# Optimization experiments

Hardware: AMD Instinct MI355X
Metric: run time of the kernel (lower is better)

## Reference

```python
import jax, jax.numpy as jnp
import numpy as np

N_IN = 8192
C_IN, C_H, C_OUT = 64, 32, 32
L = 3
GRID = 64  # parent grid extent (parents live on even coords of a 128^3 grid)


def _build_coords_and_maps():
    """Build sparse voxel coords and the 27-offset kernel map for 3x3x3 stride-1 convs."""
    rng = np.random.RandomState(0)
    pts = rng.randint(0, GRID, size=(4 * N_IN, 3))
    uniq = np.unique(pts, axis=0)
    parents = uniq[rng.permutation(uniq.shape[0])[:N_IN]] * 2  # stride-2 coords in [0,128)
    offs = np.array([[i, j, k] for i in (0, 1) for j in (0, 1) for k in (0, 1)])
    # generative conv transpose kernel=2 stride=2: child k of parent i sits at row i*8+k
    coords = (parents[:, None, :] + offs[None]).reshape(-1, 3)
    n_out = coords.shape[0]
    D = 2 * GRID
    grid = -np.ones((D, D, D), dtype=np.int64)
    grid[coords[:, 0], coords[:, 1], coords[:, 2]] = np.arange(n_out)
    k_offs = np.array([[i, j, k] for i in (-1, 0, 1) for j in (-1, 0, 1) for k in (-1, 0, 1)])
    ins, outs = [], []
    for d in k_offs:
        sh = coords + d
        valid = np.all((sh >= 0) & (sh < D), axis=1)
        j = -np.ones(n_out, dtype=np.int64)
        j[valid] = grid[sh[valid, 0], sh[valid, 1], sh[valid, 2]]
        m = j >= 0
        ins.append(j[m])
        outs.append(np.nonzero(m)[0])
    P = max(len(a) for a in ins)
    nbr_in = np.full((27, P), n_out, dtype=np.int32)   # pad -> dummy zero row
    nbr_out = np.full((27, P), n_out, dtype=np.int32)  # pad -> dummy dropped row
    for k in range(27):
        nbr_in[k, : len(ins[k])] = ins[k]
        nbr_out[k, : len(outs[k])] = outs[k]
    return jnp.asarray(nbr_in), jnp.asarray(nbr_out), n_out


def setup_inputs() -> dict:
    nbr_in, nbr_out, n_out = _build_coords_and_maps()
    key = jax.random.key(0)
    ks = jax.random.split(key, 20)
    w = lambda k, shape, fan: jax.random.normal(k, shape, jnp.float32) / np.float32(np.sqrt(fan))
    C4, C2 = C_OUT // 4, C_OUT // 2
    inp = {
        "x": jax.random.normal(ks[0], (N_IN, C_IN), jnp.float32),
        "W_up": w(ks[1], (8, C_IN, C_H), C_IN),
        "b_up": 0.01 * jax.random.normal(ks[2], (C_H,), jnp.float32),
        "W_conv": w(ks[3], (27, C_H, C_OUT), 27 * C_H),
        "b_conv": 0.01 * jax.random.normal(ks[4], (C_OUT,), jnp.float32),
        "Wb00": w(ks[5], (L, 27, C_OUT, C4), 27 * C_OUT),
        "bb00": 0.01 * jax.random.normal(ks[6], (L, C4), jnp.float32),
        "Wb01": w(ks[7], (L, 27, C4, C2), 27 * C4),
        "bb01": 0.01 * jax.random.normal(ks[8], (L, C2), jnp.float32),
        "Wb10": w(ks[9], (L, C_OUT, C4), C_OUT),
        "bb10": 0.01 * jax.random.normal(ks[10], (L, C4), jnp.float32),
        "Wb11": w(ks[11], (L, 27, C4, C4), 27 * C4),
        "bb11": 0.01 * jax.random.normal(ks[12], (L, C4), jnp.float32),
        "Wb12": w(ks[13], (L, C4, C2), C4),
        "bb12": 0.01 * jax.random.normal(ks[14], (L, C2), jnp.float32),
        "W_cls": w(ks[15], (27, C_OUT, 1), 27 * C_OUT),
        "b_cls": 0.01 * jax.random.normal(ks[16], (1,), jnp.float32),
        "nbr_in": nbr_in,
        "nbr_out": nbr_out,
        # ground-truth occupancy of out coords in target_label (precomputed set membership)
        "target": jax.random.bernoulli(ks[17], 0.5, (n_out,)),
    }
    return inp


def reference(x, W_up, b_up, W_conv, b_conv, Wb00, bb00, Wb01, bb01,
              Wb10, bb10, Wb11, bb11, Wb12, bb12, W_cls, b_cls,
              nbr_in, nbr_out, target):
    n_out = target.shape[0]
    r = jax.nn.relu

    def sconv(f, W, b):
        # 3x3x3 stride-1 sparse conv via shared kernel map: gather -> per-offset GEMM -> scatter-add
        fpad = jnp.concatenate([f, jnp.zeros((1, f.shape[1]), f.dtype)], axis=0)
        g = fpad[nbr_in]                                   # [27, P, Cin]
        contrib = jnp.einsum('kpc,kcd->kpd', g, W)         # [27, P, Cout]
        out = jnp.zeros((n_out + 1, W.shape[2]), f.dtype)
        out = out.at[nbr_out.reshape(-1)].add(contrib.reshape(-1, W.shape[2]))
        return out[:n_out] + b

    # generative transpose kernel=2 stride=2: child k of parent i -> row i*8+k
    up = (jnp.einsum('nc,kcd->nkd', x, W_up) + b_up).reshape(n_out, -1)
    out = r(sconv(r(up), W_conv, b_conv))
    for l in range(L):  # InceptionResNet blocks (PCGCv2-style)
        p0 = sconv(r(sconv(out, Wb00[l], bb00[l])), Wb01[l], bb01[l])
        p1 = r(out @ Wb10[l] + bb10[l])
        p1 = r(sconv(p1, Wb11[l], bb11[l]))
        p1 = p1 @ Wb12[l] + bb12[l]
        out = jnp.concatenate([p0, p1], axis=-1) + out
    out_cls = sconv(out, W_cls, b_cls)                     # [n_out, 1]
    score = out_cls[:, 0]
    keep = score > 0
    # topk(.,1) fallback when everything is negative
    fallback = keep | (jnp.arange(n_out) == jnp.argmax(score))
    keep = jnp.where(jnp.max(score) < 0, fallback, keep)
    # MinkowskiPruning with static shapes: zero-mask pruned rows
    out_pruned = out * keep[:, None].astype(out.dtype)
    return out_pruned, out_cls, target, keep
```

## Files before the change

### kernel.cpp

```cpp
#include <hip/hip_runtime.h>
#include <math.h>

static inline int cdiv(long long a, int b){ return (int)((a + b - 1) / b); }
#define DEVINL __device__ __forceinline__

DEVINL float4 relu4(const float* a){
  return make_float4(fmaxf(a[0],0.f), fmaxf(a[1],0.f), fmaxf(a[2],0.f), fmaxf(a[3],0.f));
}

DEVINL void load32(float* fv, const float* __restrict__ p){
#pragma unroll
  for (int q = 0; q < 8; ++q){
    float4 v = ((const float4*)p)[q];
    fv[4*q]=v.x; fv[4*q+1]=v.y; fv[4*q+2]=v.z; fv[4*q+3]=v.w;
  }
}
DEVINL void load8(float* fv, const float* __restrict__ p){
#pragma unroll
  for (int q = 0; q < 2; ++q){
    float4 v = ((const float4*)p)[q];
    fv[4*q]=v.x; fv[4*q+1]=v.y; fv[4*q+2]=v.z; fv[4*q+3]=v.w;
  }
}

DEVINL int sib_k(int o, int op){
  return 13 + 9*(((op>>2)&1) - ((o>>2)&1))
            + 3*(((op>>1)&1) - ((o>>1)&1))
            +   ((op&1) - (o&1));
}

__global__ void k_rinit(int* __restrict__ cnt, int n){
  int i = blockIdx.x*blockDim.x + threadIdx.x;
  if (i < n) cnt[i] = 0;
}

__global__ void k_rbuild(const int* __restrict__ nin, const int* __restrict__ nout,
                         int* __restrict__ cnt, int* __restrict__ rem, int P, int N){
  int p = blockIdx.x*blockDim.x + threadIdx.x;
  if (p >= 27*P) return;
  int oi = nout[p];
  if (oi >= N) return;
  int j = nin[p];
  if ((oi >> 3) == (j >> 3)) return;
  int k = p / P;
  int pos = atomicAdd(&cnt[oi], 1);
  rem[(size_t)oi*20 + pos] = (j << 5) | k;
}

__global__ __launch_bounds__(256) void k_up(const float* __restrict__ x,
    const float* __restrict__ Wup, const float* __restrict__ bup,
    float* __restrict__ f, int Nn){
  __shared__ float Ws[64*32];
  const int kk = blockIdx.y;
  for (int e = threadIdx.x*4; e < 2048; e += 1024)
    *(float4*)&Ws[e] = *(const float4*)&Wup[(size_t)kk*2048 + e];
  __syncthreads();
  int t = threadIdx.x, cg = t & 7, nr = t >> 3;
  int n = blockIdx.x*32 + nr, c0 = cg*4;
  float4 b4 = *(const float4*)(bup + c0);
  float acc[4] = {b4.x, b4.y, b4.z, b4.w};
  float xr[64];
  const float4* xp = (const float4*)(x + (size_t)n*64);
#pragma unroll
  for (int q = 0; q < 16; ++q){
    float4 v = xp[q];
    xr[4*q]=v.x; xr[4*q+1]=v.y; xr[4*q+2]=v.z; xr[4*q+3]=v.w;
  }
#pragma unroll
  for (int cc = 0; cc < 64; ++cc){
    float4 w = *(const float4*)(Ws + cc*32 + c0);
    acc[0]=fmaf(xr[cc],w.x,acc[0]); acc[1]=fmaf(xr[cc],w.y,acc[1]);
    acc[2]=fmaf(xr[cc],w.z,acc[2]); acc[3]=fmaf(xr[cc],w.w,acc[3]);
  }
  *(float4*)(f + ((size_t)n*8 + kk)*32 + c0) = relu4(acc);
}

__global__ __launch_bounds__(512) void k_conv1(const float* __restrict__ fin,
    const float* __restrict__ Wg, const float* __restrict__ bg,
    const int* __restrict__ cnt, const int* __restrict__ rem,
    float* __restrict__ fout, int N){
  __shared__ float Ws[27*32*8];
  const int cb = blockIdx.y*8;
  int t = threadIdx.x;
  for (int m = t; m < 1728; m += 512){
    int k = m >> 6, r = m & 63, cc = r >> 1, q = r & 1;
    *(float4*)&Ws[k*256 + cc*8 + q*4] =
      *(const float4*)&Wg[((size_t)(k*32 + cc))*32 + cb + q*4];
  }
  __syncthreads();
  int o = t >> 6, lane = t & 63, p = lane >> 1, cg = lane & 1;
  int base = blockIdx.x*256 + p*8;
  int row = base + o, c0 = cg*4;
  float4 b4 = *(const float4*)(bg + cb + c0);
  float acc[4] = {b4.x,b4.y,b4.z,b4.w};
  float fv[32];
#pragma unroll
  for (int op = 0; op < 8; ++op){
    int kk = sib_k(o, op);
    load32(fv, fin + (size_t)(base+op)*32);
    const float* wk = Ws + kk*256 + c0;
#pragma unroll
    for (int cc = 0; cc < 32; ++cc){
      float4 w = *(const float4*)(wk + cc*8);
      acc[0]=fmaf(fv[cc],w.x,acc[0]); acc[1]=fmaf(fv[cc],w.y,acc[1]);
      acc[2]=fmaf(fv[cc],w.z,acc[2]); acc[3]=fmaf(fv[cc],w.w,acc[3]);
    }
  }
  int nrm = cnt[row];
  for (int s = 0; s < nrm; ++s){
    int e = rem[(size_t)row*20 + s];
    int kk = e & 31, j = e >> 5;
    load32(fv, fin + (size_t)j*32);
    const float* wk = Ws + kk*256 + c0;
#pragma unroll
    for (int cc = 0; cc < 32; ++cc){
      float4 w = *(const float4*)(wk + cc*8);
      acc[0]=fmaf(fv[cc],w.x,acc[0]); acc[1]=fmaf(fv[cc],w.y,acc[1]);
      acc[2]=fmaf(fv[cc],w.z,acc[2]); acc[3]=fmaf(fv[cc],w.w,acc[3]);
    }
  }
  *(float4*)(fout + (size_t)row*32 + cb + c0) = relu4(acc);
}

__global__ __launch_bounds__(512) void k_blk_a(const float* __restrict__ fO,
    const float* __restrict__ W00, const float* __restrict__ b00,
    const float* __restrict__ W10, const float* __restrict__ b10,
    const int* __restrict__ cnt, const int* __restrict__ rem,
    float* __restrict__ a8, float* __restrict__ b8, int N){
  __shared__ float Ws[27*256 + 256];
  int t = threadIdx.x;
  for (int m = t; m < 1728; m += 512){
    int k = m >> 6, r = m & 63, cc = r >> 1, q = r & 1;
    *(float4*)&Ws[k*256 + cc*8 + q*4] = ((const float4*)W00)[m];
  }
  if (t < 64) *(float4*)&Ws[6912 + t*4] = ((const float4*)W10)[t];
  __syncthreads();
  int o = t >> 6, lane = t & 63, p = lane >> 1, cg = lane & 1;
  int base = blockIdx.x*256 + p*8;
  int row = base + o, c0 = cg*4;
  float4 b4 = *(const float4*)(b00 + c0);
  float acc[4] = {b4.x,b4.y,b4.z,b4.w};
  float fv[32];
#pragma unroll
  for (int op = 0; op < 8; ++op){
    int kk = sib_k(o, op);
    load32(fv, fO + (size_t)(base+op)*32);
    const float* wk = Ws + kk*256 + c0;
#pragma unroll
    for (int cc = 0; cc < 32; ++cc){
      float4 w = *(const float4*)(wk + cc*8);
      acc[0]=fmaf(fv[cc],w.x,acc[0]); acc[1]=fmaf(fv[cc],w.y,acc[1]);
      acc[2]=fmaf(fv[cc],w.z,acc[2]); acc[3]=fmaf(fv[cc],w.w,acc[3]);
    }
  }
  int nrm = cnt[row];
  for (int s = 0; s < nrm; ++s){
    int e = rem[(size_t)row*20 + s];
    int kk = e & 31, j = e >> 5;
    load32(fv, fO + (size_t)j*32);
    const float* wk = Ws + kk*256 + c0;
#pragma unroll
    for (int cc = 0; cc < 32; ++cc){
      float4 w = *(const float4*)(wk + cc*8);
      acc[0]=fmaf(fv[cc],w.x,acc[0]); acc[1]=fmaf(fv[cc],w.y,acc[1]);
      acc[2]=fmaf(fv[cc],w.z,acc[2]); acc[3]=fmaf(fv[cc],w.w,acc[3]);
    }
  }
  *(float4*)(a8 + (size_t)row*8 + c0) = relu4(acc);
  load32(fv, fO + (size_t)row*32);
  float4 d4 = *(const float4*)(b10 + c0);
  float accb[4] = {d4.x,d4.y,d4.z,d4.w};
#pragma unroll
  for (int cc = 0; cc < 32; ++cc){
    float4 w = *(const float4*)(Ws + 6912 + cc*8 + c0);
    accb[0]=fmaf(fv[cc],w.x,accb[0]); accb[1]=fmaf(fv[cc],w.y,accb[1]);
    accb[2]=fmaf(fv[cc],w.z,accb[2]); accb[3]=fmaf(fv[cc],w.w,accb[3]);
  }
  *(float4*)(b8 + (size_t)row*8 + c0) = relu4(accb);
}

__global__ __launch_bounds__(512) void k_blk_b(const float* __restrict__ a8,
    const float* __restrict__ b8,
    const float* __restrict__ W01, const float* __restrict__ b01,
    const float* __restrict__ W11, const float* __restrict__ b11,
    const float* __restrict__ W12, const float* __restrict__ b12,
    const int* __restrict__ cnt, const int* __restrict__ rem,
    float* __restrict__ fout, int N){
  __shared__ float Ws[27*128 + 27*64 + 128];
  int t = threadIdx.x;
  for (int m = t; m < 864; m += 512)
    ((float4*)Ws)[m] = ((const float4*)W01)[m];
  for (int m = t; m < 432; m += 512)
    ((float4*)(Ws + 3456))[m] = ((const float4*)W11)[m];
  if (t < 32) *(float4*)&Ws[5184 + t*4] = ((const float4*)W12)[t];
  __syncthreads();
  int o = t >> 6, lane = t & 63, p = lane >> 2, cg = lane & 3;
  int base = blockIdx.x*128 + p*8;
  int row = base + o, c0 = cg*4;
  float4 b4 = *(const float4*)(b01 + c0);
  float acc0[4] = {b4.x,b4.y,b4.z,b4.w};
  float t8[8];
#pragma unroll
  for (int c = 0; c < 8; ++c) t8[c] = b11[c];
  float av[8], bv[8];
#pragma unroll
  for (int op = 0; op < 8; ++op){
    int kk = sib_k(o, op);
    load8(av, a8 + (size_t)(base+op)*8);
    load8(bv, b8 + (size_t)(base+op)*8);
    const float* w01k = Ws + kk*128 + c0;
    const float* w11k = Ws + 3456 + kk*64;
#pragma unroll
    for (int cc = 0; cc < 8; ++cc){
      float4 w = *(const float4*)(w01k + cc*16);
      acc0[0]=fmaf(av[cc],w.x,acc0[0]); acc0[1]=fmaf(av[cc],w.y,acc0[1]);
      acc0[2]=fmaf(av[cc],w.z,acc0[2]); acc0[3]=fmaf(av[cc],w.w,acc0[3]);
      float4 u0 = *(const float4*)(w11k + cc*8);
      float4 u1 = *(const float4*)(w11k + cc*8 + 4);
      t8[0]=fmaf(bv[cc],u0.x,t8[0]); t8[1]=fmaf(bv[cc],u0.y,t8[1]);
      t8[2]=fmaf(bv[cc],u0.z,t8[2]); t8[3]=fmaf(bv[cc],u0.w,t8[3]);
      t8[4]=fmaf(bv[cc],u1.x,t8[4]); t8[5]=fmaf(bv[cc],u1.y,t8[5]);
      t8[6]=fmaf(bv[cc],u1.z,t8[6]); t8[7]=fmaf(bv[cc],u1.w,t8[7]);
    }
  }
  int nrm = cnt[row];
  for (int s = 0; s < nrm; ++s){
    int e = rem[(size_t)row*20 + s];
    int kk = e & 31, j = e >> 5;
    load8(av, a8 + (size_t)j*8);
    load8(bv, b8 + (size_t)j*8);
    const float* w01k = Ws + kk*128 + c0;
    const float* w11k = Ws + 3456 + kk*64;
#pragma unroll
    for (int cc = 0; cc < 8; ++cc){
      float4 w = *(const float4*)(w01k + cc*16);
      acc0[0]=fmaf(av[cc],w.x,acc0[0]); acc0[1]=fmaf(av[cc],w.y,acc0[1]);
      acc0[2]=fmaf(av[cc],w.z,acc0[2]); acc0[3]=fmaf(av[cc],w.w,acc0[3]);
      float4 u0 = *(const float4*)(w11k + cc*8);
      float4 u1 = *(const float4*)(w11k + cc*8 + 4);
      t8[0]=fmaf(bv[cc],u0.x,t8[0]); t8[1]=fmaf(bv[cc],u0.y,t8[1]);
      t8[2]=fmaf(bv[cc],u0.z,t8[2]); t8[3]=fmaf(bv[cc],u0.w,t8[3]);
      t8[4]=fmaf(bv[cc],u1.x,t8[4]); t8[5]=fmaf(bv[cc],u1.y,t8[5]);
      t8[6]=fmaf(bv[cc],u1.z,t8[6]); t8[7]=fmaf(bv[cc],u1.w,t8[7]);
    }
  }
#pragma unroll
  for (int c = 0; c < 8; ++c) t8[c] = fmaxf(t8[c], 0.f);
  float4 d4 = *(const float4*)(b12 + c0);
  float acc1[4] = {d4.x,d4.y,d4.z,d4.w};
#pragma unroll
  for (int cc = 0; cc < 8; ++cc){
    float4 w = *(const float4*)(Ws + 5184 + cc*16 + c0);
    acc1[0]=fmaf(t8[cc],w.x,acc1[0]); acc1[1]=fmaf(t8[cc],w.y,acc1[1]);
    acc1[2]=fmaf(t8[cc],w.z,acc1[2]); acc1[3]=fmaf(t8[cc],w.w,acc1[3]);
  }
  float4* o0 = (float4*)(fout + (size_t)row*32 + c0);
  float4* o1 = (float4*)(fout + (size_t)row*32 + 16 + c0);
  float4 v0 = *o0, v1 = *o1;
  v0.x+=acc0[0]; v0.y+=acc0[1]; v0.z+=acc0[2]; v0.w+=acc0[3];
  v1.x+=acc1[0]; v1.y+=acc1[1]; v1.z+=acc1[2]; v1.w+=acc1[3];
  *o0 = v0; *o1 = v1;
}

__global__ __launch_bounds__(256) void k_cls(const float* __restrict__ fO,
    const float* __restrict__ Wc, const float* __restrict__ bc,
    const int* __restrict__ cnt, const int* __restrict__ rem,
    float* __restrict__ cls, int N){
  __shared__ float Ws[27*32];
  int t = threadIdx.x;
  if (t < 216) ((float4*)Ws)[t] = ((const float4*)Wc)[t];
  __syncthreads();
  int o = blockIdx.y*4 + (t >> 6), p = t & 63;
  int base = (blockIdx.x*64 + p)*8;
  int row = base + o;
  float acc = 0.f;
  float fv[32];
#pragma unroll
  for (int op = 0; op < 8; ++op){
    int kk = sib_k(o, op);
    load32(fv, fO + (size_t)(base+op)*32);
    const float* wk = Ws + kk*32;
#pragma unroll
    for (int c4 = 0; c4 < 8; ++c4){
      float4 w = *(const float4*)(wk + c4*4);
      acc = fmaf(fv[4*c4],w.x,acc);   acc = fmaf(fv[4*c4+1],w.y,acc);
      acc = fmaf(fv[4*c4+2],w.z,acc); acc = fmaf(fv[4*c4+3],w.w,acc);
    }
  }
  int nrm = cnt[row];
  for (int s = 0; s < nrm; ++s){
    int e = rem[(size_t)row*20 + s];
    int kk = e & 31, j = e >> 5;
    load32(fv, fO + (size_t)j*32);
    const float* wk = Ws + kk*32;
#pragma unroll
    for (int c4 = 0; c4 < 8; ++c4){
      float4 w = *(const float4*)(wk + c4*4);
      acc = fmaf(fv[4*c4],w.x,acc);   acc = fmaf(fv[4*c4+1],w.y,acc);
      acc = fmaf(fv[4*c4+2],w.z,acc); acc = fmaf(fv[4*c4+3],w.w,acc);
    }
  }
  cls[row] = acc + bc[0];
}

__global__ void k_reduce1(const float* __restrict__ s, float* __restrict__ pmax,
                          int* __restrict__ pidx, int n){
  __shared__ float sm[256]; __shared__ int si[256];
  int t = threadIdx.x;
  float v = -INFINITY; int vi = 0x7fffffff;
  for (int j = blockIdx.x*256 + t; j < n; j += gridDim.x*256){
    float w = s[j];
    if (w > v){ v = w; vi = j; }
  }
  sm[t] = v; si[t] = vi; __syncthreads();
  for (int o = 128; o > 0; o >>= 1){
    if (t < o){
      if (sm[t+o] > sm[t] || (sm[t+o] == sm[t] && si[t+o] < si[t])){ sm[t]=sm[t+o]; si[t]=si[t+o]; }
    }
    __syncthreads();
  }
  if (t == 0){ pmax[blockIdx.x] = sm[0]; pidx[blockIdx.x] = si[0]; }
}

__global__ void k_reduce2(const float* __restrict__ pmax, const int* __restrict__ pidx,
                          float* __restrict__ g, int nb){
  __shared__ float sm[256]; __shared__ int si[256];
  int t = threadIdx.x;
  sm[t] = (t < nb) ? pmax[t] : -INFINITY;
  si[t] = (t < nb) ? pidx[t] : 0x7fffffff;
  __syncthreads();
  for (int o = 128; o > 0; o >>= 1){
    if (t < o){
      if (sm[t+o] > sm[t] || (sm[t+o] == sm[t] && si[t+o] < si[t])){ sm[t]=sm[t+o]; si[t]=si[t+o]; }
    }
    __syncthreads();
  }
  if (t == 0){ g[0] = sm[0]; ((int*)g)[1] = si[0]; }
}

__global__ void k_final(const float* __restrict__ out, const float* __restrict__ cls,
                        const int* __restrict__ target, const float* __restrict__ g,
                        float* __restrict__ dout, int n_out){
  int idx = blockIdx.x*blockDim.x + threadIdx.x;
  if (idx >= n_out*32) return;
  int row = idx >> 5, c = idx & 31;
  float s = cls[row];
  bool keep = s > 0.f;
  if (g[0] < 0.f) keep = keep || (row == ((const int*)g)[1]);
  float km = keep ? 1.f : 0.f;
  dout[idx] = out[idx] * km;
  if (c == 0){
    dout[(size_t)n_out*32 + row] = s;
    dout[(size_t)n_out*33 + row] = (target[row] != 0) ? 1.f : 0.f;
    dout[(size_t)n_out*34 + row] = km;
  }
}

extern "C" void kernel_launch(void* const* d_in, const int* in_sizes, int n_in,
                              void* d_out, int out_size, void* d_ws, size_t ws_size,
                              hipStream_t stream){
  const float* x      = (const float*)d_in[0];
  const float* W_up   = (const float*)d_in[1];
  const float* b_up   = (const float*)d_in[2];
  const float* W_conv = (const float*)d_in[3];
  const float* b_conv = (const float*)d_in[4];
  const float* Wb00   = (const float*)d_in[5];
  const float* bb00   = (const float*)d_in[6];
  const float* Wb01   = (const float*)d_in[7];
  const float* bb01   = (const float*)d_in[8];
  const float* Wb10   = (const float*)d_in[9];
  const float* bb10   = (const float*)d_in[10];
  const float* Wb11   = (const float*)d_in[11];
  const float* bb11   = (const float*)d_in[12];
  const float* Wb12   = (const float*)d_in[13];
  const float* bb12   = (const float*)d_in[14];
  const float* W_cls  = (const float*)d_in[15];
  const float* b_cls  = (const float*)d_in[16];
  const int*   nbr_in = (const int*)d_in[17];
  const int*   nbr_out= (const int*)d_in[18];
  const int*   target = (const int*)d_in[19];

  const int N = in_sizes[19];
  const int P = in_sizes[17] / 27;
  const int pairsT = 27 * P;
  const int Nn = N / 8;

  int*   cnt  = (int*)d_ws;
  int*   rem  = cnt + N;
  float* wsf  = (float*)(rem + (size_t)N*20);
  float* f_tmp = wsf;
  float* f_out = f_tmp + (size_t)N*32;
  float* a8    = f_out + (size_t)N*32;
  float* b8    = a8 + (size_t)N*8;
  float* cls   = b8 + (size_t)N*8;
  float* pmax  = cls + N;
  int*   pidx  = (int*)(pmax + 256);
  float* gm    = pmax + 512;

  const int B = 256;

  k_rinit<<<cdiv(N,B),B,0,stream>>>(cnt, N);
  k_rbuild<<<cdiv((long long)pairsT,B),B,0,stream>>>(nbr_in, nbr_out, cnt, rem, P, N);

  k_up<<<dim3(Nn/32,8),B,0,stream>>>(x, W_up, b_up, f_tmp, Nn);

  k_conv1<<<dim3(N/256,4),512,0,stream>>>(f_tmp, W_conv, b_conv, cnt, rem, f_out, N);

  for (int l = 0; l < 3; ++l){
    k_blk_a<<<N/256,512,0,stream>>>(f_out, Wb00 + (size_t)l*6912, bb00 + l*8,
                                    Wb10 + (size_t)l*256, bb10 + l*8, cnt, rem, a8, b8, N);
    k_blk_b<<<N/128,512,0,stream>>>(a8, b8,
                                    Wb01 + (size_t)l*3456, bb01 + l*16,
                                    Wb11 + (size_t)l*1728, bb11 + l*8,
                                    Wb12 + (size_t)l*128, bb12 + l*16,
                                    cnt, rem, f_out, N);
  }

  k_cls<<<dim3(N/512,2),B,0,stream>>>(f_out, W_cls, b_cls, cnt, rem, cls, N);

  k_reduce1<<<256,256,0,stream>>>(cls, pmax, pidx, N);
  k_reduce2<<<1,256,0,stream>>>(pmax, pidx, gm, 256);

  k_final<<<cdiv((long long)N*32,B),B,0,stream>>>(f_out, cls, target, gm, (float*)d_out, N);
}
```

Before: 217.7 us.

## Stage features in LDS and read wave-uniform repacked weights per sibling

Adds a repack kernel that reorders conv weights by (output sibling, input sibling) so each wave, with its sibling index fixed via readfirstlane, reads weights at uniform addresses that can become scalar loads. Each block stages 512 rows of features into padded LDS, so the sibling-local gathers read from shared memory instead of issuing global float4 loads. Grids are reshaped so each thread handles one row and a channel group. The costs are an extra kernel launch, a duplicated weight copy, and neighbour reads outside the sibling group that now go through uncached scalar-indexed global weights.

```diff
diff --git a/kernel.cpp b/kernel.cpp
--- a/kernel.cpp
+++ b/kernel.cpp
@@ -6,21 +6,6 @@
 
 DEVINL float4 relu4(const float* a){
   return make_float4(fmaxf(a[0],0.f), fmaxf(a[1],0.f), fmaxf(a[2],0.f), fmaxf(a[3],0.f));
-}
-
-DEVINL void load32(float* fv, const float* __restrict__ p){
-#pragma unroll
-  for (int q = 0; q < 8; ++q){
-    float4 v = ((const float4*)p)[q];
-    fv[4*q]=v.x; fv[4*q+1]=v.y; fv[4*q+2]=v.z; fv[4*q+3]=v.w;
-  }
-}
-DEVINL void load8(float* fv, const float* __restrict__ p){
-#pragma unroll
-  for (int q = 0; q < 2; ++q){
-    float4 v = ((const float4*)p)[q];
-    fv[4*q]=v.x; fv[4*q+1]=v.y; fv[4*q+2]=v.z; fv[4*q+3]=v.w;
-  }
 }
 
 DEVINL int sib_k(int o, int op){
@@ -28,6 +13,13 @@
             + 3*(((op>>1)&1) - ((o>>1)&1))
             +   ((op&1) - (o&1));
 }
+
+#define PS32 35
+#define CS32 2241
+#define LDS32 (7*CS32 + 64*PS32)
+#define PS16 19
+#define CS16 1217
+#define LDS16 (7*CS16 + 64*PS16)
 
 __global__ void k_rinit(int* __restrict__ cnt, int n){
   int i = blockIdx.x*blockDim.x + threadIdx.x;
@@ -47,258 +39,291 @@
   rem[(size_t)oi*20 + pos] = (j << 5) | k;
 }
 
-__global__ __launch_bounds__(256) void k_up(const float* __restrict__ x,
+__global__ void k_repack(const float* __restrict__ Wconv, const float* __restrict__ W00,
+                         const float* __restrict__ W01, const float* __restrict__ W11,
+                         const float* __restrict__ Wcls,
+                         float* __restrict__ Wq1, float* __restrict__ WqA,
+                         float* __restrict__ WqB0, float* __restrict__ WqB1,
+                         float* __restrict__ WqC){
+  int idx = blockIdx.x*blockDim.x + threadIdx.x;
+  if (idx < 65536){
+    int j = idx&7, cc = (idx>>3)&31, op = (idx>>8)&7, o = (idx>>11)&7, y = idx>>14;
+    int kk = sib_k(o, op);
+    Wq1[idx] = Wconv[((size_t)(kk*32+cc))*32 + y*8 + j];
+    return;
+  }
+  idx -= 65536;
+  if (idx < 49152){
+    int j = idx&3, cc = (idx>>2)&31, op = (idx>>7)&7, cg = (idx>>10)&1, o = (idx>>11)&7, l = idx>>14;
+    int kk = sib_k(o, op);
+    WqA[idx] = W00[(size_t)l*6912 + (kk*32+cc)*8 + cg*4 + j];
+    return;
+  }
+  idx -= 49152;
+  if (idx < 24576){
+    int j = idx&3, cc = (idx>>2)&7, op = (idx>>5)&7, cg = (idx>>8)&3, o = (idx>>10)&7, l = idx>>13;
+    int kk = sib_k(o, op);
+    WqB0[idx] = W01[(size_t)l*3456 + (kk*8+cc)*16 + cg*4 + j];
+    return;
+  }
+  idx -= 24576;
+  if (idx < 12288){
+    int j = idx&7, cc = (idx>>3)&7, op = (idx>>6)&7, o = (idx>>9)&7, l = idx>>12;
+    int kk = sib_k(o, op);
+    WqB1[idx] = W11[(size_t)l*1728 + (kk*8+cc)*8 + j];
+    return;
+  }
+  idx -= 12288;
+  if (idx < 2048){
+    int cc = idx&31, op = (idx>>5)&7, o = idx>>8;
+    int kk = sib_k(o, op);
+    WqC[idx] = Wcls[kk*32 + cc];
+  }
+}
+
+DEVINL void stage32(float* Ws, const float* __restrict__ src, int blk){
+  for (int m = threadIdx.x; m < 4096; m += 512){
+    int r = m >> 3, q = m & 7;
+    float4 v = ((const float4*)(src + ((size_t)(blk*512 + r))*32))[q];
+    int c = r & 7, p = r >> 3;
+    float* d = &Ws[c*CS32 + p*PS32 + q*4];
+    d[0]=v.x; d[1]=v.y; d[2]=v.z; d[3]=v.w;
+  }
+}
+
+__global__ __launch_bounds__(512) void k_up(const float* __restrict__ x,
     const float* __restrict__ Wup, const float* __restrict__ bup,
     float* __restrict__ f, int Nn){
-  __shared__ float Ws[64*32];
+  __shared__ float Ws[64*66];
   const int kk = blockIdx.y;
-  for (int e = threadIdx.x*4; e < 2048; e += 1024)
-    *(float4*)&Ws[e] = *(const float4*)&Wup[(size_t)kk*2048 + e];
-  __syncthreads();
-  int t = threadIdx.x, cg = t & 7, nr = t >> 3;
-  int n = blockIdx.x*32 + nr, c0 = cg*4;
-  float4 b4 = *(const float4*)(bup + c0);
-  float acc[4] = {b4.x, b4.y, b4.z, b4.w};
-  float xr[64];
-  const float4* xp = (const float4*)(x + (size_t)n*64);
-#pragma unroll
-  for (int q = 0; q < 16; ++q){
-    float4 v = xp[q];
-    xr[4*q]=v.x; xr[4*q+1]=v.y; xr[4*q+2]=v.z; xr[4*q+3]=v.w;
-  }
+  for (int m = threadIdx.x; m < 1024; m += 512){
+    int r = m >> 4, q = m & 15;
+    float4 v = ((const float4*)(x + ((size_t)(blockIdx.x*64 + r))*64))[q];
+    float* d = &Ws[r*66 + q*4];
+    d[0]=v.x; d[1]=v.y; d[2]=v.z; d[3]=v.w;
+  }
+  __syncthreads();
+  int w = __builtin_amdgcn_readfirstlane(threadIdx.x >> 6);
+  int nl = threadIdx.x & 63;
+  int c0 = w*4;
+  const float* wb = Wup + (size_t)kk*2048 + c0;
+  float acc[4] = {bup[c0], bup[c0+1], bup[c0+2], bup[c0+3]};
+  const float* fvp = &Ws[nl*66];
 #pragma unroll
   for (int cc = 0; cc < 64; ++cc){
-    float4 w = *(const float4*)(Ws + cc*32 + c0);
-    acc[0]=fmaf(xr[cc],w.x,acc[0]); acc[1]=fmaf(xr[cc],w.y,acc[1]);
-    acc[2]=fmaf(xr[cc],w.z,acc[2]); acc[3]=fmaf(xr[cc],w.w,acc[3]);
-  }
+    float fx = fvp[cc];
+    acc[0]=fmaf(fx, wb[cc*32+0], acc[0]); acc[1]=fmaf(fx, wb[cc*32+1], acc[1]);
+    acc[2]=fmaf(fx, wb[cc*32+2], acc[2]); acc[3]=fmaf(fx, wb[cc*32+3], acc[3]);
+  }
+  int n = blockIdx.x*64 + nl;
   *(float4*)(f + ((size_t)n*8 + kk)*32 + c0) = relu4(acc);
 }
 
 __global__ __launch_bounds__(512) void k_conv1(const float* __restrict__ fin,
-    const float* __restrict__ Wg, const float* __restrict__ bg,
+    const float* __restrict__ Wq1, const float* __restrict__ Wconv,
+    const float* __restrict__ bg,
     const int* __restrict__ cnt, const int* __restrict__ rem,
     float* __restrict__ fout, int N){
-  __shared__ float Ws[27*32*8];
-  const int cb = blockIdx.y*8;
-  int t = threadIdx.x;
-  for (int m = t; m < 1728; m += 512){
-    int k = m >> 6, r = m & 63, cc = r >> 1, q = r & 1;
-    *(float4*)&Ws[k*256 + cc*8 + q*4] =
-      *(const float4*)&Wg[((size_t)(k*32 + cc))*32 + cb + q*4];
-  }
-  __syncthreads();
-  int o = t >> 6, lane = t & 63, p = lane >> 1, cg = lane & 1;
-  int base = blockIdx.x*256 + p*8;
-  int row = base + o, c0 = cg*4;
-  float4 b4 = *(const float4*)(bg + cb + c0);
-  float acc[4] = {b4.x,b4.y,b4.z,b4.w};
-  float fv[32];
-#pragma unroll
+  __shared__ float Ws[LDS32];
+  stage32(Ws, fin, blockIdx.x);
+  __syncthreads();
+  int o = __builtin_amdgcn_readfirstlane(threadIdx.x >> 6);
+  int p = threadIdx.x & 63;
+  int row = blockIdx.x*512 + p*8 + o;
+  int cb = blockIdx.y*8;
+  const float* wb = Wq1 + (size_t)blockIdx.y*16384 + o*2048;
+  float acc[8];
+#pragma unroll
+  for (int j = 0; j < 8; ++j) acc[j] = bg[cb+j];
+#pragma unroll 1
   for (int op = 0; op < 8; ++op){
-    int kk = sib_k(o, op);
-    load32(fv, fin + (size_t)(base+op)*32);
-    const float* wk = Ws + kk*256 + c0;
+    const float* fvp = &Ws[op*CS32 + p*PS32];
+    const float* wop = wb + op*256;
 #pragma unroll
     for (int cc = 0; cc < 32; ++cc){
-      float4 w = *(const float4*)(wk + cc*8);
-      acc[0]=fmaf(fv[cc],w.x,acc[0]); acc[1]=fmaf(fv[cc],w.y,acc[1]);
-      acc[2]=fmaf(fv[cc],w.z,acc[2]); acc[3]=fmaf(fv[cc],w.w,acc[3]);
+      float fx = fvp[cc];
+#pragma unroll
+      for (int j = 0; j < 8; ++j) acc[j] = fmaf(fx, wop[cc*8+j], acc[j]);
     }
   }
   int nrm = cnt[row];
   for (int s = 0; s < nrm; ++s){
     int e = rem[(size_t)row*20 + s];
-    int kk = e & 31, j = e >> 5;
-    load32(fv, fin + (size_t)j*32);
-    const float* wk = Ws + kk*256 + c0;
+    int kk = e & 31, jr = e >> 5;
+    const float* fr = fin + (size_t)jr*32;
+    const float* wg = Wconv + (size_t)kk*1024 + cb;
 #pragma unroll
     for (int cc = 0; cc < 32; ++cc){
-      float4 w = *(const float4*)(wk + cc*8);
-      acc[0]=fmaf(fv[cc],w.x,acc[0]); acc[1]=fmaf(fv[cc],w.y,acc[1]);
-      acc[2]=fmaf(fv[cc],w.z,acc[2]); acc[3]=fmaf(fv[cc],w.w,acc[3]);
-    }
-  }
-  *(float4*)(fout + (size_t)row*32 + cb + c0) = relu4(acc);
+      float fx = fr[cc];
+#pragma unroll
+      for (int j = 0; j < 8; ++j) acc[j] = fmaf(fx, wg[cc*32+j], acc[j]);
+    }
+  }
+  *(float4*)(fout + (size_t)row*32 + cb)     = relu4(acc);
+  *(float4*)(fout + (size_t)row*32 + cb + 4) = relu4(acc+4);
 }
 
 __global__ __launch_bounds__(512) void k_blk_a(const float* __restrict__ fO,
-    const float* __restrict__ W00, const float* __restrict__ b00,
-    const float* __restrict__ W10, const float* __restrict__ b10,
+    const float* __restrict__ WqA_l, const float* __restrict__ W00_l,
+    const float* __restrict__ b00,
+    const float* __restrict__ W10_l, const float* __restrict__ b10,
     const int* __restrict__ cnt, const int* __restrict__ rem,
     float* __restrict__ a8, float* __restrict__ b8, int N){
-  __shared__ float Ws[27*256 + 256];
-  int t = threadIdx.x;
-  for (int m = t; m < 1728; m += 512){
-    int k = m >> 6, r = m & 63, cc = r >> 1, q = r & 1;
-    *(float4*)&Ws[k*256 + cc*8 + q*4] = ((const float4*)W00)[m];
-  }
-  if (t < 64) *(float4*)&Ws[6912 + t*4] = ((const float4*)W10)[t];
-  __syncthreads();
-  int o = t >> 6, lane = t & 63, p = lane >> 1, cg = lane & 1;
-  int base = blockIdx.x*256 + p*8;
-  int row = base + o, c0 = cg*4;
-  float4 b4 = *(const float4*)(b00 + c0);
-  float acc[4] = {b4.x,b4.y,b4.z,b4.w};
-  float fv[32];
-#pragma unroll
+  __shared__ float Ws[LDS32];
+  stage32(Ws, fO, blockIdx.x);
+  __syncthreads();
+  int o = __builtin_amdgcn_readfirstlane(threadIdx.x >> 6);
+  int p = threadIdx.x & 63;
+  int row = blockIdx.x*512 + p*8 + o;
+  int cg = blockIdx.y;
+  const float* wb = WqA_l + o*2048 + cg*1024;
+  float acc[4];
+#pragma unroll
+  for (int j = 0; j < 4; ++j) acc[j] = b00[cg*4+j];
+#pragma unroll 1
   for (int op = 0; op < 8; ++op){
-    int kk = sib_k(o, op);
-    load32(fv, fO + (size_t)(base+op)*32);
-    const float* wk = Ws + kk*256 + c0;
+    const float* fvp = &Ws[op*CS32 + p*PS32];
+    const float* wop = wb + op*128;
 #pragma unroll
     for (int cc = 0; cc < 32; ++cc){
-      float4 w = *(const float4*)(wk + cc*8);
-      acc[0]=fmaf(fv[cc],w.x,acc[0]); acc[1]=fmaf(fv[cc],w.y,acc[1]);
-      acc[2]=fmaf(fv[cc],w.z,acc[2]); acc[3]=fmaf(fv[cc],w.w,acc[3]);
+      float fx = fvp[cc];
+#pragma unroll
+      for (int j = 0; j < 4; ++j) acc[j] = fmaf(fx, wop[cc*4+j], acc[j]);
     }
   }
   int nrm = cnt[row];
   for (int s = 0; s < nrm; ++s){
     int e = rem[(size_t)row*20 + s];
-    int kk = e & 31, j = e >> 5;
-    load32(fv, fO + (size_t)j*32);
-    const float* wk = Ws + kk*256 + c0;
+    int kk = e & 31, jr = e >> 5;
+    const float* fr = fO + (size_t)jr*32;
+    const float* wg = W00_l + (size_t)kk*256 + cg*4;
 #pragma unroll
     for (int cc = 0; cc < 32; ++cc){
-      float4 w = *(const float4*)(wk + cc*8);
-      acc[0]=fmaf(fv[cc],w.x,acc[0]); acc[1]=fmaf(fv[cc],w.y,acc[1]);
-      acc[2]=fmaf(fv[cc],w.z,acc[2]); acc[3]=fmaf(fv[cc],w.w,acc[3]);
-    }
-  }
-  *(float4*)(a8 + (size_t)row*8 + c0) = relu4(acc);
-  load32(fv, fO + (size_t)row*32);
-  float4 d4 = *(const float4*)(b10 + c0);
-  float accb[4] = {d4.x,d4.y,d4.z,d4.w};
+      float fx = fr[cc];
+#pragma unroll
+      for (int j = 0; j < 4; ++j) acc[j] = fmaf(fx, wg[cc*8+j], acc[j]);
+    }
+  }
+  *(float4*)(a8 + (size_t)row*8 + cg*4) = relu4(acc);
+  const float* fvo = &Ws[o*CS32 + p*PS32];
+  float accb[4];
+#pragma unroll
+  for (int j = 0; j < 4; ++j) accb[j] = b10[cg*4+j];
 #pragma unroll
   for (int cc = 0; cc < 32; ++cc){
-    float4 w = *(const float4*)(Ws + 6912 + cc*8 + c0);
-    accb[0]=fmaf(fv[cc],w.x,accb[0]); accb[1]=fmaf(fv[cc],w.y,accb[1]);
-    accb[2]=fmaf(fv[cc],w.z,accb[2]); accb[3]=fmaf(fv[cc],w.w,accb[3]);
-  }
-  *(float4*)(b8 + (size_t)row*8 + c0) = relu4(accb);
+    float fx = fvo[cc];
+#pragma unroll
+    for (int j = 0; j < 4; ++j) accb[j] = fmaf(fx, W10_l[cc*8 + cg*4 + j], accb[j]);
+  }
+  *(float4*)(b8 + (size_t)row*8 + cg*4) = relu4(accb);
 }
 
 __global__ __launch_bounds__(512) void k_blk_b(const float* __restrict__ a8,
     const float* __restrict__ b8,
-    const float* __restrict__ W01, const float* __restrict__ b01,
-    const float* __restrict__ W11, const float* __restrict__ b11,
-    const float* __restrict__ W12, const float* __restrict__ b12,
+    const float* __restrict__ WqB0_l, const float* __restrict__ W01_l, const float* __restrict__ b01,
+    const float* __restrict__ WqB1_l, const float* __restrict__ W11_l, const float* __restrict__ b11,
+    const float* __restrict__ W12_l, const float* __restrict__ b12,
     const int* __restrict__ cnt, const int* __restrict__ rem,
     float* __restrict__ fout, int N){
-  __shared__ float Ws[27*128 + 27*64 + 128];
-  int t = threadIdx.x;
-  for (int m = t; m < 864; m += 512)
-    ((float4*)Ws)[m] = ((const float4*)W01)[m];
-  for (int m = t; m < 432; m += 512)
-    ((float4*)(Ws + 3456))[m] = ((const float4*)W11)[m];
-  if (t < 32) *(float4*)&Ws[5184 + t*4] = ((const float4*)W12)[t];
-  __syncthreads();
-  int o = t >> 6, lane = t & 63, p = lane >> 2, cg = lane & 3;
-  int base = blockIdx.x*128 + p*8;
-  int row = base + o, c0 = cg*4;
-  float4 b4 = *(const float4*)(b01 + c0);
-  float acc0[4] = {b4.x,b4.y,b4.z,b4.w};
-  float t8[8];
-#pragma unroll
-  for (int c = 0; c < 8; ++c) t8[c] = b11[c];
-  float av[8], bv[8];
-#pragma unroll
+  __shared__ float Ws[LDS16];
+  for (int m = threadIdx.x; m < 1024; m += 512){
+    int r = m >> 1, q = m & 1;
+    float4 va = ((const float4*)(a8 + ((size_t)(blockIdx.x*512 + r))*8))[q];
+    float4 vb = ((const float4*)(b8 + ((size_t)(blockIdx.x*512 + r))*8))[q];
+    int c = r & 7, p = r >> 3;
+    float* d = &Ws[c*CS16 + p*PS16 + q*4];
+    d[0]=va.x; d[1]=va.y; d[2]=va.z; d[3]=va.w;
+    d[8]=vb.x; d[9]=vb.y; d[10]=vb.z; d[11]=vb.w;
+  }
+  __syncthreads();
+  int o = __builtin_amdgcn_readfirstlane(threadIdx.x >> 6);
+  int p = threadIdx.x & 63;
+  int row = blockIdx.x*512 + p*8 + o;
+  int cg = blockIdx.y;
+  const float* wb0 = WqB0_l + o*1024 + cg*256;
+  const float* wb1 = WqB1_l + o*512;
+  float p0[4], t8[8];
+#pragma unroll
+  for (int j = 0; j < 4; ++j) p0[j] = b01[cg*4+j];
+#pragma unroll
+  for (int j = 0; j < 8; ++j) t8[j] = b11[j];
+#pragma unroll 1
   for (int op = 0; op < 8; ++op){
-    int kk = sib_k(o, op);
-    load8(av, a8 + (size_t)(base+op)*8);
-    load8(bv, b8 + (size_t)(base+op)*8);
-    const float* w01k = Ws + kk*128 + c0;
-    const float* w11k = Ws + 3456 + kk*64;
+    const float* avp = &Ws[op*CS16 + p*PS16];
+    const float* wop0 = wb0 + op*32;
+    const float* wop1 = wb1 + op*64;
 #pragma unroll
     for (int cc = 0; cc < 8; ++cc){
-      float4 w = *(const float4*)(w01k + cc*16);
-      acc0[0]=fmaf(av[cc],w.x,acc0[0]); acc0[1]=fmaf(av[cc],w.y,acc0[1]);
-      acc0[2]=fmaf(av[cc],w.z,acc0[2]); acc0[3]=fmaf(av[cc],w.w,acc0[3]);
-      float4 u0 = *(const float4*)(w11k + cc*8);
-      float4 u1 = *(const float4*)(w11k + cc*8 + 4);
-      t8[0]=fmaf(bv[cc],u0.x,t8[0]); t8[1]=fmaf(bv[cc],u0.y,t8[1]);
-      t8[2]=fmaf(bv[cc],u0.z,t8[2]); t8[3]=fmaf(bv[cc],u0.w,t8[3]);
-      t8[4]=fmaf(bv[cc],u1.x,t8[4]); t8[5]=fmaf(bv[cc],u1.y,t8[5]);
-      t8[6]=fmaf(bv[cc],u1.z,t8[6]); t8[7]=fmaf(bv[cc],u1.w,t8[7]);
+      float fa = avp[cc], fb = avp[cc+8];
+#pragma unroll
+      for (int j = 0; j < 4; ++j) p0[j] = fmaf(fa, wop0[cc*4+j], p0[j]);
+#pragma unroll
+      for (int j = 0; j < 8; ++j) t8[j] = fmaf(fb, wop1[cc*8+j], t8[j]);
     }
   }
   int nrm = cnt[row];
   for (int s = 0; s < nrm; ++s){
     int e = rem[(size_t)row*20 + s];
-    int kk = e & 31, j = e >> 5;
-    load8(av, a8 + (size_t)j*8);
-    load8(bv, b8 + (size_t)j*8);
-    const float* w01k = Ws + kk*128 + c0;
-    const float* w11k = Ws + 3456 + kk*64;
+    int kk = e & 31, jr = e >> 5;
+    const float* fra = a8 + (size_t)jr*8;
+    const float* frb = b8 + (size_t)jr*8;
+    const float* wg0 = W01_l + (size_t)kk*128 + cg*4;
+    const float* wg1 = W11_l + (size_t)kk*64;
 #pragma unroll
     for (int cc = 0; cc < 8; ++cc){
-      float4 w = *(const float4*)(w01k + cc*16);
-      acc0[0]=fmaf(av[cc],w.x,acc0[0]); acc0[1]=fmaf(av[cc],w.y,acc0[1]);
-      acc0[2]=fmaf(av[cc],w.z,acc0[2]); acc0[3]=fmaf(av[cc],w.w,acc0[3]);
-      float4 u0 = *(const float4*)(w11k + cc*8);
-      float4 u1 = *(const float4*)(w11k + cc*8 + 4);
-      t8[0]=fmaf(bv[cc],u0.x,t8[0]); t8[1]=fmaf(bv[cc],u0.y,t8[1]);
-      t8[2]=fmaf(bv[cc],u0.z,t8[2]); t8[3]=fmaf(bv[cc],u0.w,t8[3]);
-      t8[4]=fmaf(bv[cc],u1.x,t8[4]); t8[5]=fmaf(bv[cc],u1.y,t8[5]);
-      t8[6]=fmaf(bv[cc],u1.z,t8[6]); t8[7]=fmaf(bv[cc],u1.w,t8[7]);
-    }
-  }
-#pragma unroll
-  for (int c = 0; c < 8; ++c) t8[c] = fmaxf(t8[c], 0.f);
-  float4 d4 = *(const float4*)(b12 + c0);
-  float acc1[4] = {d4.x,d4.y,d4.z,d4.w};
+      float fa = fra[cc], fb = frb[cc];
+#pragma unroll
+      for (int j = 0; j < 4; ++j) p0[j] = fmaf(fa, wg0[cc*16+j], p0[j]);
+#pragma unroll
+      for (int j = 0; j < 8; ++j) t8[j] = fmaf(fb, wg1[cc*8+j], t8[j]);
+    }
+  }
+#pragma unroll
+  for (int j = 0; j < 8; ++j) t8[j] = fmaxf(t8[j], 0.f);
+  float p1[4];
+#pragma unroll
+  for (int j = 0; j < 4; ++j) p1[j] = b12[cg*4+j];
 #pragma unroll
   for (int cc = 0; cc < 8; ++cc){
-    float4 w = *(const float4*)(Ws + 5184 + cc*16 + c0);
-    acc1[0]=fmaf(t8[cc],w.x,acc1[0]); acc1[1]=fmaf(t8[cc],w.y,acc1[1]);
-    acc1[2]=fmaf(t8[cc],w.z,acc1[2]); acc1[3]=fmaf(t8[cc],w.w,acc1[3]);
-  }
-  float4* o0 = (float4*)(fout + (size_t)row*32 + c0);
-  float4* o1 = (float4*)(fout + (size_t)row*32 + 16 + c0);
+#pragma unroll
+    for (int j = 0; j < 4; ++j) p1[j] = fmaf(t8[cc], W12_l[cc*16 + cg*4 + j], p1[j]);
+  }
+  float4* o0 = (float4*)(fout + (size_t)row*32 + cg*4);
+  float4* o1 = (float4*)(fout + (size_t)row*32 + 16 + cg*4);
   float4 v0 = *o0, v1 = *o1;
-  v0.x+=acc0[0]; v0.y+=acc0[1]; v0.z+=acc0[2]; v0.w+=acc0[3];
-  v1.x+=acc1[0]; v1.y+=acc1[1]; v1.z+=acc1[2]; v1.w+=acc1[3];
+  v0.x+=p0[0]; v0.y+=p0[1]; v0.z+=p0[2]; v0.w+=p0[3];
+  v1.x+=p1[0]; v1.y+=p1[1]; v1.z+=p1[2]; v1.w+=p1[3];
   *o0 = v0; *o1 = v1;
 }
 
-__global__ __launch_bounds__(256) void k_cls(const float* __restrict__ fO,
-    const float* __restrict__ Wc, const float* __restrict__ bc,
+__global__ __launch_bounds__(512) void k_cls(const float* __restrict__ fO,
+    const float* __restrict__ WqC, const float* __restrict__ Wcls,
+    const float* __restrict__ bc,
     const int* __restrict__ cnt, const int* __restrict__ rem,
     float* __restrict__ cls, int N){
-  __shared__ float Ws[27*32];
-  int t = threadIdx.x;
-  if (t < 216) ((float4*)Ws)[t] = ((const float4*)Wc)[t];
-  __syncthreads();
-  int o = blockIdx.y*4 + (t >> 6), p = t & 63;
-  int base = (blockIdx.x*64 + p)*8;
-  int row = base + o;
+  __shared__ float Ws[LDS32];
+  stage32(Ws, fO, blockIdx.x);
+  __syncthreads();
+  int o = __builtin_amdgcn_readfirstlane(threadIdx.x >> 6);
+  int p = threadIdx.x & 63;
+  int row = blockIdx.x*512 + p*8 + o;
+  const float* wb = WqC + o*256;
   float acc = 0.f;
-  float fv[32];
-#pragma unroll
+#pragma unroll 1
   for (int op = 0; op < 8; ++op){
-    int kk = sib_k(o, op);
-    load32(fv, fO + (size_t)(base+op)*32);
-    const float* wk = Ws + kk*32;
-#pragma unroll
-    for (int c4 = 0; c4 < 8; ++c4){
-      float4 w = *(const float4*)(wk + c4*4);
-      acc = fmaf(fv[4*c4],w.x,acc);   acc = fmaf(fv[4*c4+1],w.y,acc);
-      acc = fmaf(fv[4*c4+2],w.z,acc); acc = fmaf(fv[4*c4+3],w.w,acc);
-    }
+    const float* fvp = &Ws[op*CS32 + p*PS32];
+    const float* wop = wb + op*32;
+#pragma unroll
+    for (int cc = 0; cc < 32; ++cc) acc = fmaf(fvp[cc], wop[cc], acc);
   }
   int nrm = cnt[row];
   for (int s = 0; s < nrm; ++s){
     int e = rem[(size_t)row*20 + s];
-    int kk = e & 31, j = e >> 5;
-    load32(fv, fO + (size_t)j*32);
-    const float* wk = Ws + kk*32;
-#pragma unroll
-    for (int c4 = 0; c4 < 8; ++c4){
-      float4 w = *(const float4*)(wk + c4*4);
-      acc = fmaf(fv[4*c4],w.x,acc);   acc = fmaf(fv[4*c4+1],w.y,acc);
-      acc = fmaf(fv[4*c4+2],w.z,acc); acc = fmaf(fv[4*c4+3],w.w,acc);
-    }
+    int kk = e & 31, jr = e >> 5;
+    const float* fr = fO + (size_t)jr*32;
+    const float* wg = Wcls + kk*32;
+#pragma unroll
+    for (int cc = 0; cc < 32; ++cc) acc = fmaf(fr[cc], wg[cc], acc);
   }
   cls[row] = acc + bc[0];
 }
@@ -387,8 +412,12 @@
 
   int*   cnt  = (int*)d_ws;
   int*   rem  = cnt + N;
-  float* wsf  = (float*)(rem + (size_t)N*20);
-  float* f_tmp = wsf;
+  float* Wq1  = (float*)(rem + (size_t)N*20);
+  float* WqA  = Wq1 + 65536;
+  float* WqB0 = WqA + 49152;
+  float* WqB1 = WqB0 + 24576;
+  float* WqC  = WqB1 + 12288;
+  float* f_tmp = WqC + 2048;
   float* f_out = f_tmp + (size_t)N*32;
   float* a8    = f_out + (size_t)N*32;
   float* b8    = a8 + (size_t)N*8;
@@ -401,22 +430,23 @@
 
   k_rinit<<<cdiv(N,B),B,0,stream>>>(cnt, N);
   k_rbuild<<<cdiv((long long)pairsT,B),B,0,stream>>>(nbr_in, nbr_out, cnt, rem, P, N);
-
-  k_up<<<dim3(Nn/32,8),B,0,stream>>>(x, W_up, b_up, f_tmp, Nn);
-
-  k_conv1<<<dim3(N/256,4),512,0,stream>>>(f_tmp, W_conv, b_conv, cnt, rem, f_out, N);
+  k_repack<<<600,B,0,stream>>>(W_conv, Wb00, Wb01, Wb11, W_cls, Wq1, WqA, WqB0, WqB1, WqC);
+
+  k_up<<<dim3(Nn/64,8),512,0,stream>>>(x, W_up, b_up, f_tmp, Nn);
+
+  k_conv1<<<dim3(N/512,4),512,0,stream>>>(f_tmp, Wq1, W_conv, b_conv, cnt, rem, f_out, N);
 
   for (int l = 0; l < 3; ++l){
-    k_blk_a<<<N/256,512,0,stream>>>(f_out, Wb00 + (size_t)l*6912, bb00 + l*8,
-                                    Wb10 + (size_t)l*256, bb10 + l*8, cnt, rem, a8, b8, N);
-    k_blk_b<<<N/128,512,0,stream>>>(a8, b8,
-                                    Wb01 + (size_t)l*3456, bb01 + l*16,
-                                    Wb11 + (size_t)l*1728, bb11 + l*8,
-                                    Wb12 + (size_t)l*128, bb12 + l*16,
-                                    cnt, rem, f_out, N);
-  }
-
-  k_cls<<<dim3(N/512,2),B,0,stream>>>(f_out, W_cls, b_cls, cnt, rem, cls, N);
+    k_blk_a<<<dim3(N/512,2),512,0,stream>>>(f_out,
+        WqA + (size_t)l*16384, Wb00 + (size_t)l*6912, bb00 + l*8,
+        Wb10 + (size_t)l*256, bb10 + l*8, cnt, rem, a8, b8, N);
+    k_blk_b<<<dim3(N/512,4),512,0,stream>>>(a8, b8,
+        WqB0 + (size_t)l*8192, Wb01 + (size_t)l*3456, bb01 + l*16,
+        WqB1 + (size_t)l*4096, Wb11 + (size_t)l*1728, bb11 + l*8,
+        Wb12 + (size_t)l*128, bb12 + l*16, cnt, rem, f_out, N);
+  }
+
+  k_cls<<<N/512,512,0,stream>>>(f_out, WqC, W_cls, b_cls, cnt, rem, cls, N);
 
   k_reduce1<<<256,256,0,stream>>>(cls, pmax, pidx, N);
   k_reduce2<<<1,256,0,stream>>>(pmax, pidx, gm, 256);
```

New measurement: 370.2 us. 1.7x slower.
